# Kernel optimization log

Measured on AMD Instinct MI355X. Metric: run time of the kernel, lower is better.

Reference implementation:

```python
import jax, jax.numpy as jnp
import numpy as np

P, B, H, IN, L = 64, 256, 512, 2, 2


def setup_inputs() -> dict:
    key = jax.random.key(0)
    ks = jax.random.split(key, 16)
    s = 1.0 / np.sqrt(H)
    inp = {
        'input_traces': jax.random.normal(ks[0], (B, P, IN), jnp.float32),
        'h0': jax.random.normal(ks[1], (P, L, B, H), jnp.float32) * 0.1,
        'c0': jax.random.normal(ks[2], (P, L, B, H), jnp.float32) * 0.1,
        # layer 0 LSTM params (PyTorch layout: [4H, in] with gate order i,f,g,o)
        'w_ih0': jax.random.uniform(ks[3], (4 * H, IN), jnp.float32, -s, s),
        'w_hh0': jax.random.uniform(ks[4], (4 * H, H), jnp.float32, -s, s),
        'b_ih0': jax.random.uniform(ks[5], (4 * H,), jnp.float32, -s, s),
        'b_hh0': jax.random.uniform(ks[6], (4 * H,), jnp.float32, -s, s),
        # layer 1 LSTM params
        'w_ih1': jax.random.uniform(ks[7], (4 * H, H), jnp.float32, -s, s),
        'w_hh1': jax.random.uniform(ks[8], (4 * H, H), jnp.float32, -s, s),
        'b_ih1': jax.random.uniform(ks[9], (4 * H,), jnp.float32, -s, s),
        'b_hh1': jax.random.uniform(ks[10], (4 * H,), jnp.float32, -s, s),
    }
    return inp


def _lstm_forward(input_traces, h0, c0, params):
    # Fuse pedestrian and batch dims into one big batch PB = P*B; the original
    # loops over pedestrians calling the SAME LSTM weights, so this is exact.
    x = jnp.transpose(input_traces, (1, 0, 2)).reshape(P * B, IN)  # [PB, 2]
    h = jnp.transpose(h0, (1, 0, 2, 3)).reshape(L, P * B, H)       # [L, PB, H]
    c = jnp.transpose(c0, (1, 0, 2, 3)).reshape(L, P * B, H)
    h_next, c_next = [], []
    for l in range(L):
        wi, wh, bi, bh = params[l]
        gates = x @ wi.T + bi + h[l] @ wh.T + bh                   # [PB, 4H]
        ig, fg, gg, og = jnp.split(gates, 4, axis=-1)
        ig, fg, og = jax.nn.sigmoid(ig), jax.nn.sigmoid(fg), jax.nn.sigmoid(og)
        gg = jnp.tanh(gg)
        c_new = fg * c[l] + ig * gg
        h_new = og * jnp.tanh(c_new)
        h_next.append(h_new)
        c_next.append(c_new)
        x = h_new
    out = x.reshape(P, B, H).transpose(1, 0, 2)                    # [B, P, H]
    hn = jnp.stack(h_next).reshape(L, P, B, H).transpose(1, 0, 2, 3)
    cn = jnp.stack(c_next).reshape(L, P, B, H).transpose(1, 0, 2, 3)
    return out, hn, cn


def reference(input_traces, h0, c0, w_ih0, w_hh0, b_ih0, b_hh0,
              w_ih1, w_hh1, b_ih1, b_hh1):
    params = [(w_ih0, w_hh0, b_ih0, b_hh0), (w_ih1, w_hh1, b_ih1, b_hh1)]
    return _lstm_forward(input_traces, h0, c0, params)
```

## Files before the change

kernel.cpp:

```cpp
#include <hip/hip_runtime.h>
#include <hip/hip_bf16.h>

#define PP 64
#define BB 256
#define HH 512
#define MM (PP * BB)

#define HN_BASE (BB * PP * HH)
#define CN_BASE (HN_BASE + PP * 2 * BB * HH)

#define TILE8K 8192
#define WS_A0   0ull
#define WS_A1A  16777216ull
#define WS_A1B  33554432ull
#define WS_W0   50331648ull
#define WS_W1A  52428800ull
#define WS_W1B  54525952ull
#define WS_NEED 56623104ull

typedef __attribute__((ext_vector_type(8))) short bf16x8;
typedef __attribute__((ext_vector_type(4))) float floatx4;

__device__ __forceinline__ float sigf(float x) { return 1.0f / (1.0f + __expf(-x)); }
__device__ __forceinline__ float tanh_(float x) { return 2.0f / (1.0f + __expf(-2.0f * x)) - 1.0f; }

__device__ __forceinline__ short f2bf(float f) {
  unsigned u = __float_as_uint(f);
  u = (u + 0x7FFFu + ((u >> 16) & 1u)) >> 16;
  return (short)u;
}

template <typename T>
__device__ __forceinline__ float tofl(T v);
template <> __device__ __forceinline__ float tofl<float>(float v) { return v; }
template <> __device__ __forceinline__ float tofl<__hip_bfloat16>(__hip_bfloat16 v) { return __bfloat162float(v); }

template <typename T>
__device__ __forceinline__ T fromfl(float v);
template <> __device__ __forceinline__ float fromfl<float>(float v) { return v; }
template <> __device__ __forceinline__ __hip_bfloat16 fromfl<__hip_bfloat16>(float v) { return __float2bfloat16(v); }

template <typename T>
__device__ __forceinline__ bf16x8 load8(const T* p);
template <> __device__ __forceinline__ bf16x8 load8<__hip_bfloat16>(const __hip_bfloat16* p) {
  return *(const bf16x8*)p;
}
template <> __device__ __forceinline__ bf16x8 load8<float>(const float* p) {
  float4 f0 = *(const float4*)p;
  float4 f1 = *((const float4*)p + 1);
  bf16x8 v;
  v[0] = f2bf(f0.x); v[1] = f2bf(f0.y); v[2] = f2bf(f0.z); v[3] = f2bf(f0.w);
  v[4] = f2bf(f1.x); v[5] = f2bf(f1.y); v[6] = f2bf(f1.z); v[7] = f2bf(f1.w);
  return v;
}

__device__ __forceinline__ bool detect_f32(const void* w_ih0) {
  const unsigned short* p = (const unsigned short*)w_ih0;
  int l = threadIdx.x & 63;
  unsigned short a = p[2 * l], b = p[2 * l + 1];
  int big = ((a & 0x7F80) >= 0x3F80) || ((b & 0x7F80) >= 0x3F80);
  return __any(big);
}

__device__ __forceinline__ void gload16(void* ldsp, const void* g) {
  __builtin_amdgcn_global_load_lds(
      (const __attribute__((address_space(1))) unsigned int*)g,
      (__attribute__((address_space(3))) unsigned int*)ldsp, 16, 0, 0);
}


template <typename T>
__device__ __forceinline__ void prep_A_body(const T* __restrict__ h0, char* __restrict__ ws) {
  const int pb = blockIdx.x, kt = blockIdx.y, l = blockIdx.z;
  char* dst = ws + (l ? WS_A1B : WS_A0) + ((size_t)(pb * 16 + kt)) * TILE8K;
  const int ped = pb >> 1, bh = pb & 1;
  const T* src = h0 + ((size_t)(ped * 2 + l) * 256) * 512;
  const int tid = threadIdx.x;
#pragma unroll
  for (int i = 0; i < 2; ++i) {
    int idx = i * 256 + tid;
    int ln  = idx & 63;
    int rb  = idx >> 6;
    int row = bh * 128 + rb * 16 + (ln & 15);
    int col = kt * 32 + (ln >> 4) * 8;
    *(bf16x8*)(dst + (size_t)idx * 16) = load8<T>(src + (size_t)row * 512 + col);
  }
}

__global__ void __launch_bounds__(256) prep_A_k(const void* h0, const void* det, void* ws) {
  if (detect_f32(det)) prep_A_body<float>((const float*)h0, (char*)ws);
  else prep_A_body<__hip_bfloat16>((const __hip_bfloat16*)h0, (char*)ws);
}

template <typename T>
__device__ __forceinline__ void prep_W_body(const T* __restrict__ w0, const T* __restrict__ w1a,
                                            const T* __restrict__ w1b, char* __restrict__ ws) {
  const int m = blockIdx.x >> 4, hb = blockIdx.x & 15, kt = blockIdx.y;
  const T* src = (m == 0) ? w0 : (m == 1 ? w1a : w1b);
  const size_t base = (m == 0) ? WS_W0 : (m == 1 ? WS_W1A : WS_W1B);
  char* dst = ws + base + ((size_t)(hb * 16 + kt)) * TILE8K;
  const int tid = threadIdx.x;
#pragma unroll
  for (int i = 0; i < 2; ++i) {
    int idx = i * 256 + tid;
    int ln  = idx & 63;
    int rb  = idx >> 6;
    int g   = rb >> 1, half = rb & 1;
    int j   = g * 512 + hb * 32 + half * 16 + (ln & 15);
    int col = kt * 32 + (ln >> 4) * 8;
    *(bf16x8*)(dst + (size_t)idx * 16) = load8<T>(src + (size_t)j * 512 + col);
  }
}

__global__ void __launch_bounds__(256) prep_W_k(const void* w0, const void* w1a, const void* w1b,
                                                const void* det, void* ws) {
  if (detect_f32(det)) prep_W_body<float>((const float*)w0, (const float*)w1a, (const float*)w1b, (char*)ws);
  else prep_W_body<__hip_bfloat16>((const __hip_bfloat16*)w0, (const __hip_bfloat16*)w1a,
                                   (const __hip_bfloat16*)w1b, (char*)ws);
}

template <typename T, int LAYER>
__device__ __forceinline__ void lstm_dma_body(
    const T* __restrict__ xin, const T* __restrict__ c0,
    const T* __restrict__ wih, const T* __restrict__ bih, const T* __restrict__ bhh,
    T* __restrict__ out, char* __restrict__ ws, char* lds)
{
  const int tid  = threadIdx.x;
  const int hb   = blockIdx.x;
  const int nb   = blockIdx.y;
  const int lane = tid & 63;
  const int wid  = tid >> 6;
  const int quad = lane >> 4;
  const int lrow = lane & 15;
  const int p0   = nb >> 1;

  floatx4 acc[4][4];
#pragma unroll
  for (int g = 0; g < 4; ++g)
#pragma unroll
    for (int mi = 0; mi < 4; ++mi)
#pragma unroll
      for (int q = 0; q < 4; ++q) acc[g][mi][q] = 0.0f;

  const int a_rb0  = (wid >> 1) * 4;
  const int w_half = wid & 1;

  constexpr int KITERS = (LAYER == 0) ? 16 : 32;

  auto stage = [&](int buf, int kt) {
    const char *at, *wt;
    if (LAYER == 0) {
      at = ws + WS_A0  + ((size_t)(nb * 16 + kt)) * TILE8K;
      wt = ws + WS_W0  + ((size_t)(hb * 16 + kt)) * TILE8K;
    } else if (kt < 16) {
      at = ws + WS_A1A + ((size_t)(nb * 16 + kt)) * TILE8K;
      wt = ws + WS_W1A + ((size_t)(hb * 16 + kt)) * TILE8K;
    } else {
      at = ws + WS_A1B + ((size_t)(nb * 16 + kt - 16)) * TILE8K;
      wt = ws + WS_W1B + ((size_t)(hb * 16 + kt - 16)) * TILE8K;
    }
    char* la = lds + buf * 16384;
    char* lw = la + TILE8K;
#pragma unroll
    for (int i = 0; i < 2; ++i) {
      int base = (i * 4 + wid) * 1024;
      int off  = base + lane * 16;
      gload16(la + base, at + off);
      gload16(lw + base, wt + off);
    }
  };

  stage(0, 0);
  __syncthreads();

#pragma unroll
  for (int kt = 0; kt < KITERS; ++kt) {
    const int cur = kt & 1;
    if (kt + 1 < KITERS) stage(cur ^ 1, kt + 1);

    const char* la = lds + cur * 16384;
    const char* lw = la + TILE8K;
    bf16x8 aF[4], wF[4];
#pragma unroll
    for (int mi = 0; mi < 4; ++mi)
      aF[mi] = *(const bf16x8*)(la + ((a_rb0 + mi) * 1024) + lane * 16);
#pragma unroll
    for (int g = 0; g < 4; ++g)
      wF[g] = *(const bf16x8*)(lw + ((g * 2 + w_half) * 1024) + lane * 16);
#pragma unroll
    for (int g = 0; g < 4; ++g)
#pragma unroll
      for (int mi = 0; mi < 4; ++mi)
        acc[g][mi] = __builtin_amdgcn_mfma_f32_16x16x32_bf16(
            aF[mi], wF[g], acc[g][mi], 0, 0, 0);

    __syncthreads();
  }

  const int hloc = hb * 32 + w_half * 16 + lrow;
  float bias[4], wx0[4], wx1[4];
#pragma unroll
  for (int g = 0; g < 4; ++g) {
    int j = g * 512 + hloc;
    bias[g] = tofl<T>(bih[j]) + tofl<T>(bhh[j]);
    if (LAYER == 0) {
      wx0[g] = tofl<T>(wih[j * 2]);
      wx1[g] = tofl<T>(wih[j * 2 + 1]);
    }
  }
  const int crow0 = (p0 * 2 + LAYER) * 256;
  const int kt_h = hloc >> 5;
  const int qd_h = (hloc >> 3) & 3;
  const int el_h = hloc & 7;
  char* a1a_tile = ws + WS_A1A + ((size_t)(nb * 16 + kt_h)) * TILE8K;

#pragma unroll
  for (int mi = 0; mi < 4; ++mi) {
#pragma unroll
    for (int r = 0; r < 4; ++r) {
      int rr = (wid >> 1) * 64 + mi * 16 + quad * 4 + r;
      int b  = ((nb & 1) << 7) + rr;
      float gv0 = acc[0][mi][r] + bias[0];
      float gv1 = acc[1][mi][r] + bias[1];
      float gv2 = acc[2][mi][r] + bias[2];
      float gv3 = acc[3][mi][r] + bias[3];
      if (LAYER == 0) {
        float x0 = tofl<T>(xin[(b * 64 + p0) * 2]);
        float x1 = tofl<T>(xin[(b * 64 + p0) * 2 + 1]);
        gv0 += x0 * wx0[0] + x1 * wx1[0];
        gv1 += x0 * wx0[1] + x1 * wx1[1];
        gv2 += x0 * wx0[2] + x1 * wx1[2];
        gv3 += x0 * wx0[3] + x1 * wx1[3];
      }
      float ig = sigf(gv0), fg = sigf(gv1);
      float gg = tanh_(gv2), og = sigf(gv3);
      size_t ro = ((size_t)(crow0 + b)) * 512 + hloc;
      float co   = tofl<T>(c0[ro]);
      float cnew = fg * co + ig * gg;
      float hnew = og * tanh_(cnew);
      out[HN_BASE + ro] = fromfl<T>(hnew);
      out[CN_BASE + ro] = fromfl<T>(cnew);
      if (LAYER == 0) {
        int slot = ((rr >> 4) * 64) + qd_h * 16 + (rr & 15);
        *(short*)(a1a_tile + (size_t)slot * 16 + el_h * 2) = f2bf(hnew);
      }
      if (LAYER == 1)
        out[(size_t)(b * 64 + p0) * 512 + hloc] = fromfl<T>(hnew);
    }
  }
}

template <int LAYER>
__global__ void __launch_bounds__(256, 4)
lstm_dma(const void* xin, const void* c0, const void* wih,
         const void* bih, const void* bhh, const void* det,
         void* out, void* ws)
{
  __shared__ __align__(16) char lds[2 * 16384];
  if (detect_f32(det)) {
    lstm_dma_body<float, LAYER>((const float*)xin, (const float*)c0, (const float*)wih,
                                (const float*)bih, (const float*)bhh,
                                (float*)out, (char*)ws, lds);
  } else {
    lstm_dma_body<__hip_bfloat16, LAYER>((const __hip_bfloat16*)xin, (const __hip_bfloat16*)c0,
                                         (const __hip_bfloat16*)wih, (const __hip_bfloat16*)bih,
                                         (const __hip_bfloat16*)bhh,
                                         (__hip_bfloat16*)out, (char*)ws, lds);
  }
}

template <typename T, int LAYER>
__device__ __forceinline__ void lstm_body(
    const T* __restrict__ xin, const T* __restrict__ h0, const T* __restrict__ c0,
    const T* __restrict__ wih, const T* __restrict__ whh,
    const T* __restrict__ bih, const T* __restrict__ bhh,
    T* out, __hip_bfloat16* ldsA, __hip_bfloat16* ldsW)
{
  const int tid  = threadIdx.x;
  const int nb   = blockIdx.x;
  const int hb   = blockIdx.y;
  const int lane = tid & 63;
  const int wid  = tid >> 6;
  const int quad = lane >> 4;
  const int lrow = lane & 15;
  const int p0   = nb >> 1;

  floatx4 acc[4][4];
#pragma unroll
  for (int g = 0; g < 4; ++g)
#pragma unroll
    for (int mi = 0; mi < 4; ++mi)
#pragma unroll
      for (int q = 0; q < 4; ++q) acc[g][mi][q] = 0.0f;

  int arow[4], wrow[4];
#pragma unroll
  for (int mi = 0; mi < 4; ++mi) arow[mi] = (wid >> 1) * 64 + mi * 16 + lrow;
#pragma unroll
  for (int g = 0; g < 4; ++g) wrow[g] = g * 32 + (wid & 1) * 16 + lrow;

  const int sr = tid >> 3;
  const int sc = tid & 7;
  const int KITERS = (LAYER == 0) ? 8 : 16;

  for (int kt = 0; kt < KITERS; ++kt) {
    bf16x8 ra[4], rw[4];
#pragma unroll
    for (int round = 0; round < 4; ++round) {
      int r = sr + round * 32;
      int b = ((nb & 1) << 7) + r;
      const T* srcA;
      if (LAYER == 0) {
        srcA = h0 + ((size_t)((p0 * 2) * 256 + b)) * 512 + kt * 64 + sc * 8;
      } else {
        if (kt < 8)
          srcA = out + HN_BASE + ((size_t)((p0 * 2) * 256 + b)) * 512 + kt * 64 + sc * 8;
        else
          srcA = h0 + ((size_t)((p0 * 2 + 1) * 256 + b)) * 512 + (kt - 8) * 64 + sc * 8;
      }
      ra[round] = load8<T>(srcA);

      int j = (r >> 5) * 512 + hb * 32 + (r & 31);
      const T* srcW;
      if (LAYER == 0) {
        srcW = whh + (size_t)j * 512 + kt * 64 + sc * 8;
      } else {
        if (kt < 8) srcW = wih + (size_t)j * 512 + kt * 64 + sc * 8;
        else        srcW = whh + (size_t)j * 512 + (kt - 8) * 64 + sc * 8;
      }
      rw[round] = load8<T>(srcW);
    }

    __syncthreads();
#pragma unroll
    for (int round = 0; round < 4; ++round) {
      int r = sr + round * 32;
      int p = sc ^ (r & 7);
      *(bf16x8*)((char*)ldsA + r * 128 + p * 16) = ra[round];
      *(bf16x8*)((char*)ldsW + r * 128 + p * 16) = rw[round];
    }
    __syncthreads();

#pragma unroll
    for (int ks = 0; ks < 2; ++ks) {
      bf16x8 aF[4], wF[4];
#pragma unroll
      for (int mi = 0; mi < 4; ++mi) {
        int ch = (ks * 4 + quad) ^ (arow[mi] & 7);
        aF[mi] = *(const bf16x8*)((const char*)ldsA + arow[mi] * 128 + ch * 16);
      }
#pragma unroll
      for (int g = 0; g < 4; ++g) {
        int ch = (ks * 4 + quad) ^ (wrow[g] & 7);
        wF[g] = *(const bf16x8*)((const char*)ldsW + wrow[g] * 128 + ch * 16);
      }
#pragma unroll
      for (int g = 0; g < 4; ++g)
#pragma unroll
        for (int mi = 0; mi < 4; ++mi)
          acc[g][mi] = __builtin_amdgcn_mfma_f32_16x16x32_bf16(
              aF[mi], wF[g], acc[g][mi], 0, 0, 0);
    }
  }

  const int hloc = hb * 32 + (wid & 1) * 16 + lrow;
  float bias[4], wx0[4], wx1[4];
#pragma unroll
  for (int g = 0; g < 4; ++g) {
    int j = g * 512 + hloc;
    bias[g] = tofl<T>(bih[j]) + tofl<T>(bhh[j]);
    if (LAYER == 0) {
      wx0[g] = tofl<T>(wih[j * 2]);
      wx1[g] = tofl<T>(wih[j * 2 + 1]);
    }
  }
  const int crow0 = (p0 * 2 + LAYER) * 256;
#pragma unroll
  for (int mi = 0; mi < 4; ++mi) {
#pragma unroll
    for (int r = 0; r < 4; ++r) {
      int b = ((nb & 1) << 7) + (wid >> 1) * 64 + mi * 16 + quad * 4 + r;
      float gv0 = acc[0][mi][r] + bias[0];
      float gv1 = acc[1][mi][r] + bias[1];
      float gv2 = acc[2][mi][r] + bias[2];
      float gv3 = acc[3][mi][r] + bias[3];
      if (LAYER == 0) {
        float x0 = tofl<T>(xin[(b * 64 + p0) * 2]);
        float x1 = tofl<T>(xin[(b * 64 + p0) * 2 + 1]);
        gv0 += x0 * wx0[0] + x1 * wx1[0];
        gv1 += x0 * wx0[1] + x1 * wx1[1];
        gv2 += x0 * wx0[2] + x1 * wx1[2];
        gv3 += x0 * wx0[3] + x1 * wx1[3];
      }
      float ig = sigf(gv0), fg = sigf(gv1);
      float gg = tanh_(gv2), og = sigf(gv3);
      size_t ro = ((size_t)(crow0 + b)) * 512 + hloc;
      float co   = tofl<T>(c0[ro]);
      float cnew = fg * co + ig * gg;
      float hnew = og * tanh_(cnew);
      out[HN_BASE + ro] = fromfl<T>(hnew);
      out[CN_BASE + ro] = fromfl<T>(cnew);
      if (LAYER == 1)
        out[(size_t)(b * 64 + p0) * 512 + hloc] = fromfl<T>(hnew);
    }
  }
}

template <int LAYER>
__global__ void __launch_bounds__(256)
lstm_layer(const void* xin, const void* h0, const void* c0,
           const void* wih, const void* whh, const void* bih, const void* bhh,
           const void* w_ih0_detect, void* out)
{
  __shared__ __align__(16) __hip_bfloat16 ldsA[128 * 64];
  __shared__ __align__(16) __hip_bfloat16 ldsW[128 * 64];
  if (detect_f32(w_ih0_detect)) {
    lstm_body<float, LAYER>((const float*)xin, (const float*)h0, (const float*)c0,
                            (const float*)wih, (const float*)whh,
                            (const float*)bih, (const float*)bhh,
                            (float*)out, ldsA, ldsW);
  } else {
    lstm_body<__hip_bfloat16, LAYER>((const __hip_bfloat16*)xin, (const __hip_bfloat16*)h0,
                                     (const __hip_bfloat16*)c0, (const __hip_bfloat16*)wih,
                                     (const __hip_bfloat16*)whh, (const __hip_bfloat16*)bih,
                                     (const __hip_bfloat16*)bhh, (__hip_bfloat16*)out,
                                     ldsA, ldsW);
  }
}

extern "C" void kernel_launch(void* const* d_in, const int* in_sizes, int n_in,
                              void* d_out, int out_size, void* d_ws, size_t ws_size,
                              hipStream_t stream) {
  dim3 block(256);
  if (d_ws != nullptr && ws_size >= WS_NEED) {
    prep_A_k<<<dim3(128, 16, 2), block, 0, stream>>>(d_in[1], d_in[3], d_ws);
    prep_W_k<<<dim3(48, 16), block, 0, stream>>>(d_in[4], d_in[7], d_in[8], d_in[3], d_ws);
    dim3 grid(HH / 32, MM / 128);
    lstm_dma<0><<<grid, block, 0, stream>>>(d_in[0], d_in[2], d_in[3],
                                            d_in[5], d_in[6], d_in[3], d_out, d_ws);
    lstm_dma<1><<<grid, block, 0, stream>>>(d_in[0], d_in[2], d_in[3],
                                            d_in[9], d_in[10], d_in[3], d_out, d_ws);
  } else {
    dim3 grid(MM / 128, HH / 32);
    lstm_layer<0><<<grid, block, 0, stream>>>(d_in[0], d_in[1], d_in[2],
                                              d_in[3], d_in[4], d_in[5], d_in[6],
                                              d_in[3], d_out);
    lstm_layer<1><<<grid, block, 0, stream>>>(d_in[0], d_in[1], d_in[2],
                                              d_in[7], d_in[8], d_in[9], d_in[10],
                                              d_in[3], d_out);
  }
}
```

Before: 457.7 us.

## Coalesce h-panel repacking via LDS and remap workgroups across XCDs

```diff
diff --git a/kernel.cpp b/kernel.cpp
--- a/kernel.cpp
+++ b/kernel.cpp
@@ -68,28 +68,57 @@
       (__attribute__((address_space(3))) unsigned int*)ldsp, 16, 0, 0);
 }
 
-
 template <typename T>
-__device__ __forceinline__ void prep_A_body(const T* __restrict__ h0, char* __restrict__ ws) {
-  const int pb = blockIdx.x, kt = blockIdx.y, l = blockIdx.z;
-  char* dst = ws + (l ? WS_A1B : WS_A0) + ((size_t)(pb * 16 + kt)) * TILE8K;
-  const int ped = pb >> 1, bh = pb & 1;
-  const T* src = h0 + ((size_t)(ped * 2 + l) * 256) * 512;
+__device__ __forceinline__ void prep_panel_body(const T* __restrict__ src, char* __restrict__ dst,
+                                                char* lds) {
   const int tid = threadIdx.x;
-#pragma unroll
-  for (int i = 0; i < 2; ++i) {
-    int idx = i * 256 + tid;
-    int ln  = idx & 63;
-    int rb  = idx >> 6;
-    int row = bh * 128 + rb * 16 + (ln & 15);
-    int col = kt * 32 + (ln >> 4) * 8;
-    *(bf16x8*)(dst + (size_t)idx * 16) = load8<T>(src + (size_t)row * 512 + col);
-  }
-}
-
-__global__ void __launch_bounds__(256) prep_A_k(const void* h0, const void* det, void* ws) {
-  if (detect_f32(det)) prep_A_body<float>((const float*)h0, (char*)ws);
-  else prep_A_body<__hip_bfloat16>((const __hip_bfloat16*)h0, (char*)ws);
+  for (int cc = 0; cc < 8; ++cc) {
+#pragma unroll
+    for (int i = 0; i < 8; ++i) {
+      int idx = i * 256 + tid;
+      int row = idx >> 4;
+      int c4  = idx & 15;
+      int c   = c4 * 4;
+      const T* p = src + (size_t)row * 512 + cc * 64 + c;
+      short4 s;
+      if constexpr (sizeof(T) == 4) {
+        float4 f = *(const float4*)p;
+        s.x = f2bf(f.x); s.y = f2bf(f.y); s.z = f2bf(f.z); s.w = f2bf(f.w);
+      } else {
+        s = *(const short4*)p;
+      }
+      int tile = c >> 5;
+      int qd   = (c & 31) >> 3;
+      int e0   = c & 7;
+      int rb   = row >> 4, lr = row & 15;
+      *(short4*)(lds + tile * 8192 + ((rb * 64 + qd * 16 + lr) * 16) + e0 * 2) = s;
+    }
+    __syncthreads();
+#pragma unroll
+    for (int i = 0; i < 4; ++i) {
+      int idx = i * 256 + tid;
+      int kt  = cc * 2 + (idx >> 9);
+      *(bf16x8*)(dst + (size_t)kt * TILE8K + (size_t)(idx & 511) * 16) =
+          *(const bf16x8*)(lds + (size_t)idx * 16);
+    }
+    __syncthreads();
+  }
+}
+
+__global__ void __launch_bounds__(256)
+prep_panel_k(const void* tensor, const void* det, void* ws,
+             unsigned long long off0, unsigned long long off1, int is_hn) {
+  const int pb = blockIdx.x, l = blockIdx.y;
+  __shared__ __align__(16) char lds[16384];
+  char* dst = (char*)ws + (l ? off1 : off0) + (size_t)pb * 16 * TILE8K;
+  const size_t srcoff = (((size_t)(pb >> 1) * 2 + l) * 256 + (size_t)(pb & 1) * 128) * 512;
+  if (detect_f32(det)) {
+    const float* t = (const float*)tensor + (is_hn ? (size_t)HN_BASE : 0);
+    prep_panel_body<float>(t + srcoff, dst, lds);
+  } else {
+    const __hip_bfloat16* t = (const __hip_bfloat16*)tensor + (is_hn ? (size_t)HN_BASE : 0);
+    prep_panel_body<__hip_bfloat16>(t + srcoff, dst, lds);
+  }
 }
 
 template <typename T>
@@ -126,8 +155,10 @@
     T* __restrict__ out, char* __restrict__ ws, char* lds)
 {
   const int tid  = threadIdx.x;
-  const int hb   = blockIdx.x;
-  const int nb   = blockIdx.y;
+  const int wg   = blockIdx.x;
+  const int wgid = (wg & 7) * 256 + (wg >> 3);
+  const int hb   = wgid & 15;
+  const int nb   = wgid >> 4;
   const int lane = tid & 63;
   const int wid  = tid >> 6;
   const int quad = lane >> 4;
@@ -209,10 +240,6 @@
     }
   }
   const int crow0 = (p0 * 2 + LAYER) * 256;
-  const int kt_h = hloc >> 5;
-  const int qd_h = (hloc >> 3) & 3;
-  const int el_h = hloc & 7;
-  char* a1a_tile = ws + WS_A1A + ((size_t)(nb * 16 + kt_h)) * TILE8K;
 
 #pragma unroll
   for (int mi = 0; mi < 4; ++mi) {
@@ -240,10 +267,6 @@
       float hnew = og * tanh_(cnew);
       out[HN_BASE + ro] = fromfl<T>(hnew);
       out[CN_BASE + ro] = fromfl<T>(cnew);
-      if (LAYER == 0) {
-        int slot = ((rr >> 4) * 64) + qd_h * 16 + (rr & 15);
-        *(short*)(a1a_tile + (size_t)slot * 16 + el_h * 2) = f2bf(hnew);
-      }
       if (LAYER == 1)
         out[(size_t)(b * 64 + p0) * 512 + hloc] = fromfl<T>(hnew);
     }
@@ -433,11 +456,14 @@
                               hipStream_t stream) {
   dim3 block(256);
   if (d_ws != nullptr && ws_size >= WS_NEED) {
-    prep_A_k<<<dim3(128, 16, 2), block, 0, stream>>>(d_in[1], d_in[3], d_ws);
+    prep_panel_k<<<dim3(128, 2), block, 0, stream>>>(d_in[1], d_in[3], d_ws,
+                                                     WS_A0, WS_A1B, 0);
     prep_W_k<<<dim3(48, 16), block, 0, stream>>>(d_in[4], d_in[7], d_in[8], d_in[3], d_ws);
-    dim3 grid(HH / 32, MM / 128);
+    dim3 grid(2048);
     lstm_dma<0><<<grid, block, 0, stream>>>(d_in[0], d_in[2], d_in[3],
                                             d_in[5], d_in[6], d_in[3], d_out, d_ws);
+    prep_panel_k<<<dim3(128, 1), block, 0, stream>>>(d_out, d_in[3], d_ws,
+                                                     WS_A1A, WS_A1A, 1);
     lstm_dma<1><<<grid, block, 0, stream>>>(d_in[0], d_in[2], d_in[3],
                                             d_in[9], d_in[10], d_in[3], d_out, d_ws);
   } else {
```

Measured after the change: 483.2 us. +5.6%, slower.
